# Kernel optimization log

Measured on AMD Instinct MI355X. Metric: run time of the kernel, lower is better.

## Reference

```python
import jax, jax.numpy as jnp
import numpy as np

EPS = 1e-5
POOL_R, POOL_T, SCALE = 5, 7, 0.125  # pool_r, pool_t, 1/pool_stride


def conv_bn_relu(x, W, b, gamma, beta, pad):
    # Conv2d(bias) + BatchNorm2d (training-mode batch stats, biased var) + ReLU
    y = jax.lax.conv_general_dilated(x, W, (1, 1), [(pad, pad), (pad, pad)],
                                     dimension_numbers=('NCHW', 'OIHW', 'NCHW'))
    y = y + b[None, :, None, None]
    mean = y.mean(axis=(0, 2, 3))
    var = y.var(axis=(0, 2, 3))
    y = (y - mean[None, :, None, None]) * jax.lax.rsqrt(var + EPS)[None, :, None, None]
    y = y * gamma[None, :, None, None] + beta[None, :, None, None]
    return jax.nn.relu(y)


def linear_bn_relu(x, W, b, gamma, beta):
    # LinearBlock: Linear + BatchNorm (over batch dim) + ReLU
    y = x @ W.T + b
    mean = y.mean(axis=0)
    var = y.var(axis=0)
    y = (y - mean) * jax.lax.rsqrt(var + EPS) * gamma + beta
    return jax.nn.relu(y)


def _hat_int(x):
    # Antiderivative of the triangular (bilinear) hat kernel at offset x.
    u = jnp.clip(x, -1.0, 1.0)
    return jnp.where(u <= 0, 0.5 * (1.0 + u) ** 2, 0.5 + u - 0.5 * u ** 2)


def prroi_pool(feat, rois, ph, pw, scale):
    # Exact PrRoIPool2D. feat: [B,C,H,W]; rois: [B,N,4] xyxy in image coords.
    # Bilinear interp is a sum of separable hat kernels at integer grid points, so the
    # exact bin integral factorizes into per-axis hat-integral weights Wx, Wy.
    B, C, H, W = feat.shape
    x1, y1, x2, y2 = [rois[..., i] * scale for i in range(4)]
    bw = (x2 - x1) / pw   # [B,N]
    bh = (y2 - y1) / ph
    qx = jnp.arange(pw, dtype=feat.dtype)
    qy = jnp.arange(ph, dtype=feat.dtype)
    xs_lo = x1[..., None] + qx * bw[..., None]   # [B,N,Pw]
    ys_lo = y1[..., None] + qy * bh[..., None]   # [B,N,Ph]
    gw = jnp.arange(W, dtype=feat.dtype)
    gh = jnp.arange(H, dtype=feat.dtype)
    Wx = _hat_int(xs_lo[..., None] + bw[..., None, None] - gw) - _hat_int(xs_lo[..., None] - gw)  # [B,N,Pw,W]
    Wy = _hat_int(ys_lo[..., None] + bh[..., None, None] - gh) - _hat_int(ys_lo[..., None] - gh)  # [B,N,Ph,H]
    out = jnp.einsum('bchw,bnph,bnqw->bncpq', feat, Wy, Wx)
    area = (bw * bh)[:, :, None, None, None]
    return jnp.where(area > 0, out / jnp.maximum(area, 1e-12), 0.0)  # [B,N,C,Ph,Pw]


def _forward(feat1, feat2, bb1, proposals2,
             w_c1r, b_c1r, g_c1r, be_c1r,
             w_c1t, b_c1t, g_c1t, be_c1t,
             w_c2t, b_c2t, g_c2t, be_c2t,
             w_f1r, b_f1r, g_f1r, be_f1r,
             w_f2r, b_f2r, g_f2r, be_f2r,
             w_f1rt, b_f1rt, g_f1rt, be_f1rt,
             w_f2rt, b_f2rt, g_f2rt, be_f2rt,
             w_iou, b_iou):
    S = feat2.shape[0]
    N = proposals2.shape[2]
    # --- get_modulation ---
    c3_r = conv_bn_relu(feat1, w_c1r, b_c1r, g_c1r, be_c1r, 1)
    bb = bb1[0]  # [S,4] xywh -> xyxy
    roi_r = jnp.concatenate([bb[:, :2], bb[:, :2] + bb[:, 2:4]], axis=1)[:, None, :]
    pooled_r = prroi_pool(c3_r, roi_r, POOL_R, POOL_R, SCALE)[:, 0]   # [S,256,5,5]
    m = conv_bn_relu(pooled_r, w_f1r, b_f1r, g_f1r, be_f1r, 0)        # [S,1024,1,1]
    m = conv_bn_relu(m, w_f2r, b_f2r, g_f2r, be_f2r, 0)               # [S,256,1,1]
    modulation = m.reshape(S, -1)                                     # [S,256]
    # --- get_iou_feat ---
    c3_t = conv_bn_relu(conv_bn_relu(feat2, w_c1t, b_c1t, g_c1t, be_c1t, 1),
                        w_c2t, b_c2t, g_c2t, be_c2t, 1)
    # --- predict_iou ---
    c3_t_att = c3_t * modulation[:, :, None, None]
    props = proposals2[0]  # [S,N,4] xywh -> xyxy
    rois_t = jnp.concatenate([props[..., :2], props[..., :2] + props[..., 2:4]], axis=-1)
    pooled_t = prroi_pool(c3_t_att, rois_t, POOL_T, POOL_T, SCALE)    # [S,N,256,7,7]
    x = pooled_t.reshape(S * N, -1)
    x = linear_bn_relu(x, w_f1rt, b_f1rt, g_f1rt, be_f1rt)
    x = linear_bn_relu(x, w_f2rt, b_f2rt, g_f2rt, be_f2rt)
    iou = x @ w_iou.T + b_iou
    return iou.reshape(1, S, N)  # (num_images, num_sequences, num_proposals)


def setup_inputs() -> dict:
    key = jax.random.key(0)
    ks = jax.random.split(key, 8)
    S, C, Hf, Wf, N = 64, 256, 36, 36, 16
    inp = {}
    inp['feat1'] = jax.random.normal(ks[0], (S, C, Hf, Wf), jnp.float32)
    inp['feat2'] = jax.random.normal(ks[1], (S, C, Hf, Wf), jnp.float32)
    xy1 = jax.random.uniform(ks[2], (1, S, 2), minval=20.0, maxval=180.0)
    wh1 = jax.random.uniform(ks[3], (1, S, 2), minval=40.0, maxval=100.0)
    inp['bb1'] = jnp.concatenate([xy1, wh1], axis=-1).astype(jnp.float32)
    xy2 = jax.random.uniform(ks[4], (1, S, N, 2), minval=20.0, maxval=180.0)
    wh2 = jax.random.uniform(ks[5], (1, S, N, 2), minval=40.0, maxval=100.0)
    inp['proposals2'] = jnp.concatenate([xy2, wh2], axis=-1).astype(jnp.float32)

    def kaiming(k, shape):
        fan_in = int(np.prod(shape[1:]))
        return (jax.random.normal(k, shape) * np.sqrt(2.0 / fan_in)).astype(jnp.float32)

    kp = jax.random.split(ks[6], 8)
    specs = [('c1r', (256, C, 3, 3), kp[0]), ('c1t', (256, C, 3, 3), kp[1]),
             ('c2t', (256, 256, 3, 3), kp[2]), ('f1r', (1024, 256, 5, 5), kp[3]),
             ('f2r', (256, 1024, 1, 1), kp[4]), ('f1rt', (1024, 256 * 7 * 7), kp[5]),
             ('f2rt', (1024, 1024), kp[6])]
    for name, shape, k in specs:
        inp['w_' + name] = kaiming(k, shape)
        oc = shape[0]
        inp['b_' + name] = jnp.zeros(oc, jnp.float32)
        inp['g_' + name] = jnp.ones(oc, jnp.float32)
        inp['be_' + name] = jnp.zeros(oc, jnp.float32)
    inp['w_iou'] = kaiming(kp[7], (1, 1024))
    inp['b_iou'] = jnp.zeros(1, jnp.float32)
    return inp


def reference(feat1, feat2, bb1, proposals2,
              w_c1r, b_c1r, g_c1r, be_c1r,
              w_c1t, b_c1t, g_c1t, be_c1t,
              w_c2t, b_c2t, g_c2t, be_c2t,
              w_f1r, b_f1r, g_f1r, be_f1r,
              w_f2r, b_f2r, g_f2r, be_f2r,
              w_f1rt, b_f1rt, g_f1rt, be_f1rt,
              w_f2rt, b_f2rt, g_f2rt, be_f2rt,
              w_iou, b_iou):
    return _forward(feat1, feat2, bb1, proposals2,
                    w_c1r, b_c1r, g_c1r, be_c1r,
                    w_c1t, b_c1t, g_c1t, be_c1t,
                    w_c2t, b_c2t, g_c2t, be_c2t,
                    w_f1r, b_f1r, g_f1r, be_f1r,
                    w_f2r, b_f2r, g_f2r, be_f2r,
                    w_f1rt, b_f1rt, g_f1rt, be_f1rt,
                    w_f2rt, b_f2rt, g_f2rt, be_f2rt,
                    w_iou, b_iou)
```

## Files before the change

### kernel.cpp

```cpp
#include <hip/hip_runtime.h>
#include <cstddef>


typedef _Float16 f16;
typedef __attribute__((ext_vector_type(4))) _Float16 f16x4;
typedef __attribute__((ext_vector_type(8))) _Float16 f16x8;
typedef __attribute__((ext_vector_type(4))) float f32x4;

__device__ __forceinline__ void gload16(const void* g, void* l) {
  __builtin_amdgcn_global_load_lds((const __attribute__((address_space(1))) void*)g,
                                   (__attribute__((address_space(3))) void*)l, 16, 0, 0);
}

#define WAITB(N) asm volatile("s_waitcnt vmcnt(" #N ")\n\ts_barrier" ::: "memory")
#define LGKB()   asm volatile("s_waitcnt lgkmcnt(0)\n\ts_barrier" ::: "memory")

static __device__ __forceinline__ float hat_int(float x) {
  float u = fminf(1.f, fmaxf(-1.f, x));
  float a = 0.5f * (1.f + u) * (1.f + u);
  float b = 0.5f + u - 0.5f * u * u;
  return (u <= 0.f) ? a : b;
}

static __device__ __forceinline__ size_t pk_off(int row, int k, int K) {
  return (size_t)(row >> 7) * ((size_t)K * 128) + (size_t)(k >> 5) * 4096
       + (size_t)((((k >> 3) & 3) * 128 + (row & 127)) * 8 + (k & 7));
}

__global__ void k_zero(float4* __restrict__ p, int n4) {
  int i = blockIdx.x * 256 + threadIdx.x;
  if (i < n4) p[i] = float4{0.f, 0.f, 0.f, 0.f};
}

__global__ void k_border(f16* __restrict__ FT) {
  const int img = blockIdx.x;
  f16* base = FT + (size_t)img * 32 * 1444 * 8;
  for (int i = threadIdx.x; i < 148 * 256; i += 256) {
    int b = i >> 8, c = i & 255;
    int r, cc;
    if (b < 38)       { r = 0;          cc = b; }
    else if (b < 76)  { r = 37;         cc = b - 38; }
    else if (b < 112) { r = b - 76 + 1; cc = 0; }
    else              { r = b - 112 + 1; cc = 37; }
    base[((size_t)(c >> 3) * 1444 + r * 38 + cc) * 8 + (c & 7)] = (f16)0.f;
  }
}

__global__ void k_pad(const float* __restrict__ src, f16* __restrict__ FT) {
  const int img = blockIdx.x, h = blockIdx.y, c = threadIdx.x;
  const float* sp = src + ((size_t)img * 256 + c) * 1296 + h * 36;
  f16* op = FT + (((size_t)img * 32 + (c >> 3)) * 1444 + (h + 1) * 38 + 1) * 8 + (c & 7);
#pragma unroll 4
  for (int w = 0; w < 36; ++w) op[w * 8] = (f16)sp[w];
}

__global__ void k_pad2(const f16* __restrict__ yH, f16* __restrict__ FT,
                       const float* __restrict__ mean, const float* __restrict__ istd,
                       const float* __restrict__ g, const float* __restrict__ be) {
  const int img = blockIdx.x, h = blockIdx.y, c = threadIdx.x;
  const float sc = istd[c] * g[c];
  const float sh = be[c] - mean[c] * sc;
  const f16* sp = yH + ((size_t)img * 1296 + h * 36) * 256 + c;
  f16* op = FT + (((size_t)img * 32 + (c >> 3)) * 1444 + (h + 1) * 38 + 1) * 8 + (c & 7);
#pragma unroll 4
  for (int w = 0; w < 36; ++w) {
    float v = fmaxf(fmaf((float)sp[w * 256], sc, sh), 0.f);
    op[w * 8] = (f16)v;
  }
}

__global__ void k_pack_wc(const float* __restrict__ w, f16* __restrict__ dst) {
  int i = blockIdx.x * 256 + threadIdx.x;
  int oct = i / 294912;
  int r = i - oct * 294912;
  int ks = r >> 12;
  int r2 = r & 4095;
  int koct = r2 >> 10;
  int r3 = r2 & 1023;
  int row = r3 >> 3, kj = r3 & 7;
  int k = ks * 32 + koct * 8 + kj;
  int t = k >> 8, c = k & 255;
  int oc = oct * 128 + row;
  dst[i] = (f16)w[(oc * 256 + c) * 9 + t];
}

__global__ __launch_bounds__(256) void k_packx_h(
    const f16* __restrict__ src, f16* __restrict__ dst, int M, int K) {
  __shared__ f16 sT[128][264];
  const int k0 = blockIdx.x * 256, r0 = blockIdx.y * 128;
  const int t = threadIdx.x;
  const int rl = t >> 5, kk = (t & 31) * 8;
  for (int rnd = 0; rnd < 16; ++rnd) {
    const int row_l = rl + rnd * 8;
    const int row = r0 + row_l;
    if (row < M) {
      f16x8 v = *reinterpret_cast<const f16x8*>(src + (size_t)row * K + k0 + kk);
      *reinterpret_cast<f16x8*>(&sT[row_l][kk]) = v;
    }
  }
  __syncthreads();
  const size_t base = (size_t)(r0 >> 7) * ((size_t)K * 128) + (size_t)(k0 >> 5) * 4096;
#pragma unroll
  for (int cs = 0; cs < 8; ++cs) {
#pragma unroll
    for (int half = 0; half < 2; ++half) {
      const int e = half * 256 + t;
      const int koct = e >> 7, row_l = e & 127;
      if (r0 + row_l < M) {
        f16x8 v = *reinterpret_cast<const f16x8*>(&sT[row_l][cs * 32 + koct * 8]);
        *reinterpret_cast<f16x8*>(dst + base + (size_t)cs * 4096 + e * 8) = v;
      }
    }
  }
}

__global__ __launch_bounds__(256) void k_packx_f(
    const float* __restrict__ src, f16* __restrict__ dst, int M, int K) {
  __shared__ f16 sT[128][264];
  const int k0 = blockIdx.x * 256, r0 = blockIdx.y * 128;
  const int t = threadIdx.x;
  const int rl = t >> 5, kk = (t & 31) * 8;
  for (int rnd = 0; rnd < 16; ++rnd) {
    const int row_l = rl + rnd * 8;
    const int row = r0 + row_l;
    if (row < M) {
      const float4* sp = reinterpret_cast<const float4*>(src + (size_t)row * K + k0 + kk);
      float4 a = sp[0], b = sp[1];
      f16* o = &sT[row_l][kk];
      o[0] = (f16)a.x; o[1] = (f16)a.y; o[2] = (f16)a.z; o[3] = (f16)a.w;
      o[4] = (f16)b.x; o[5] = (f16)b.y; o[6] = (f16)b.z; o[7] = (f16)b.w;
    }
  }
  __syncthreads();
  const size_t base = (size_t)(r0 >> 7) * ((size_t)K * 128) + (size_t)(k0 >> 5) * 4096;
#pragma unroll
  for (int cs = 0; cs < 8; ++cs) {
#pragma unroll
    for (int half = 0; half < 2; ++half) {
      const int e = half * 256 + t;
      const int koct = e >> 7, row_l = e & 127;
      if (r0 + row_l < M) {
        f16x8 v = *reinterpret_cast<const f16x8*>(&sT[row_l][cs * 32 + koct * 8]);
        *reinterpret_cast<f16x8*>(dst + base + (size_t)cs * 4096 + e * 8) = v;
      }
    }
  }
}

__global__ __launch_bounds__(256) void k_conv_mfma(
    const f16* __restrict__ Wpk, const f16* __restrict__ FT2,
    const float* __restrict__ bias, f16* __restrict__ yH) {
  __shared__ f16x8 sA[1536];
  __shared__ f16x8 sB[1536];
  const int bid = blockIdx.x;
  const int orig = (bid & 7) * 176 + (bid >> 3);
  const int img = orig / 22;
  const int rem = orig - img * 22;
  const int oct = rem / 11;
  const int pt  = rem - oct * 11;
  const int m0 = oct * 128;
  const int p0 = pt * 128;
  const int tid = threadIdx.x;
  const int lane = tid & 63;
  const int wv = tid >> 6;
  const int wr = wv >> 1, wc = wv & 1;

  const f16* aBase = Wpk + (size_t)oct * 294912 + wv * 1024 + lane * 8;
  const f16* ftImg = FT2 + (size_t)img * 32 * 1444 * 8;
  int pos0 = p0 + lane;
  int pc0 = min(pos0, 1295);
  int pc1 = min(pos0 + 64, 1295);
  int pb0 = (pc0 / 36) * 38 + (pc0 % 36);
  int pb1 = (pc1 / 36) * 38 + (pc1 % 36);

  const int loff = wv * 2048 + lane * 16;

  auto stage = [&](int buf, int ks) {
    const int t = ks >> 3;
    const int dy = t / 3, dx = t - dy * 3;
    const int cs = ks & 7;
    const int dyx = dy * 38 + dx;
    char* lA = (char*)sA + buf * 8192 + loff;
    char* lB = (char*)sB + buf * 8192 + loff;
    const f16* ap = aBase + (size_t)ks * 4096;
    const f16* bp = ftImg + ((size_t)(cs * 4 + wv) * 1444 + dyx) * 8;
    gload16(ap, lA);
    gload16(ap + 512, lA + 1024);
    gload16(bp + pb0 * 8, lB);
    gload16(bp + pb1 * 8, lB + 1024);
  };

  f32x4 acc[4][4] = {};
  const int fidxA = ((lane >> 4) << 7) + wr * 64 + (lane & 15);
  const int fidxB = ((lane >> 4) << 7) + wc * 64 + (lane & 15);

  stage(0, 0); stage(1, 1); stage(2, 2);
  int cur = 0;
  for (int ks = 0; ks < 72; ++ks) {
    const int r = 71 - ks;
    if (r >= 2)      WAITB(8);
    else if (r == 1) WAITB(4);
    else             WAITB(0);
    const int base = cur * 512;
    f16x8 af[4], bf[4];
#pragma unroll
    for (int i = 0; i < 4; ++i) {
      af[i] = sA[base + fidxA + i * 16];
      bf[i] = sB[base + fidxB + i * 16];
    }
#pragma unroll
    for (int i = 0; i < 4; ++i)
#pragma unroll
      for (int j = 0; j < 4; ++j)
        acc[i][j] = __builtin_amdgcn_mfma_f32_16x16x32_f16(af[i], bf[j], acc[i][j], 0, 0, 0);
    LGKB();
    if (ks + 3 < 72) stage(cur, ks + 3);
    cur = (cur == 2) ? 0 : cur + 1;
  }

  const int colb = p0 + wc * 64 + (lane & 15);
  const int rowb = m0 + wr * 64 + ((lane >> 4) << 2);
  f16* yb = yH + (size_t)img * 1296 * 256;
#pragma unroll
  for (int i = 0; i < 4; ++i) {
    const int oc0 = rowb + i * 16;
    float b0 = bias[oc0], b1 = bias[oc0 + 1], b2 = bias[oc0 + 2], b3 = bias[oc0 + 3];
#pragma unroll
    for (int j = 0; j < 4; ++j) {
      const int col = colb + j * 16;
      if (col < 1296) {
        f16x4 v;
        v[0] = (f16)(acc[i][j][0] + b0);
        v[1] = (f16)(acc[i][j][1] + b1);
        v[2] = (f16)(acc[i][j][2] + b2);
        v[3] = (f16)(acc[i][j][3] + b3);
        *reinterpret_cast<f16x4*>(yb + (size_t)col * 256 + oc0) = v;
      }
    }
  }
}

__global__ __launch_bounds__(256) void k_gemm_f16pk(
    const f16* __restrict__ Apk, const f16* __restrict__ Bpk,
    float* __restrict__ part, int K, int Nout, int stepsPerZ, int mrows) {
  __shared__ f16x8 sA[1536];
  __shared__ f16x8 sB[1536];
  const int nt = blockIdx.x, mt = blockIdx.y, z = blockIdx.z;
  const int tid = threadIdx.x;
  const int lane = tid & 63;
  const int wv = tid >> 6;
  const int wr = wv >> 1, wc = wv & 1;

  const f16* aC = Apk + (size_t)mt * K * 128 + wv * 1024 + lane * 8;
  const f16* bC = Bpk + (size_t)nt * K * 128 + wv * 1024 + lane * 8;
  const int loff = wv * 2048 + lane * 16;

  auto stage = [&](int buf, int ks) {
    char* lA = (char*)sA + buf * 8192 + loff;
    char* lB = (char*)sB + buf * 8192 + loff;
    const f16* ap = aC + (size_t)ks * 4096;
    const f16* bp = bC + (size_t)ks * 4096;
    gload16(ap, lA);
    gload16(ap + 512, lA + 1024);
    gload16(bp, lB);
    gload16(bp + 512, lB + 1024);
  };

  f32x4 acc[4][4] = {};
  const int fidxA = ((lane >> 4) << 7) + wr * 64 + (lane & 15);
  const int fidxB = ((lane >> 4) << 7) + wc * 64 + (lane & 15);

  const int ks0 = z * stepsPerZ;
  stage(0, ks0); stage(1, ks0 + 1); stage(2, ks0 + 2);
  int cur = 0;
  for (int i = 0; i < stepsPerZ; ++i) {
    const int r = stepsPerZ - 1 - i;
    if (r >= 2)      WAITB(8);
    else if (r == 1) WAITB(4);
    else             WAITB(0);
    const int base = cur * 512;
    f16x8 af[4], bf[4];
#pragma unroll
    for (int j = 0; j < 4; ++j) {
      af[j] = sA[base + fidxA + j * 16];
      bf[j] = sB[base + fidxB + j * 16];
    }
#pragma unroll
    for (int ii = 0; ii < 4; ++ii)
#pragma unroll
      for (int jj = 0; jj < 4; ++jj)
        acc[ii][jj] = __builtin_amdgcn_mfma_f32_16x16x32_f16(af[ii], bf[jj], acc[ii][jj], 0, 0, 0);
    LGKB();
    if (i + 3 < stepsPerZ) stage(cur, ks0 + i + 3);
    cur = (cur == 2) ? 0 : cur + 1;
  }

  const size_t zoff = (size_t)z * mrows * Nout;
  const int colb = nt * 128 + wc * 64 + (lane & 15);
  const int rowb = mt * 128 + wr * 64 + ((lane >> 4) << 2);
#pragma unroll
  for (int i = 0; i < 4; ++i)
#pragma unroll
    for (int j = 0; j < 4; ++j)
#pragma unroll
      for (int r = 0; r < 4; ++r)
        part[zoff + (size_t)(rowb + i * 16 + r) * Nout + colb + j * 16] = acc[i][j][r];
}

__global__ void k_reduce(const float* __restrict__ part, const float* __restrict__ bias,
                         float* __restrict__ out, int mrows, int Mout, int Nout, int sk) {
  int i = blockIdx.x * 256 + threadIdx.x;
  if (i >= Mout * Nout) return;
  int row = i / Nout, col = i - row * Nout;
  float s = bias[col];
  for (int z = 0; z < sk; ++z)
    s += part[(size_t)z * mrows * Nout + (size_t)row * Nout + col];
  out[i] = s;
}

__global__ void k_chan_stats_hwc(const f16* __restrict__ yH,
                                 float* __restrict__ psum, float* __restrict__ psq) {
  const int z = blockIdx.x, c = threadIdx.x;
  const f16* p = yH + (size_t)z * 256 * 256 + c;
  float s = 0.f, ss = 0.f;
#pragma unroll 4
  for (int i = 0; i < 256; ++i) {
    float v = (float)p[(size_t)i * 256];
    s += v; ss += v * v;
  }
  psum[z * 256 + c] = s;
  psq[z * 256 + c] = ss;
}

__global__ void k_chan_stats_hwc_final(const float* __restrict__ psum,
                                       const float* __restrict__ psq,
                                       float* __restrict__ mean, float* __restrict__ istd) {
  const int c = threadIdx.x;
  float s = 0.f, ss = 0.f;
  for (int z = 0; z < 324; ++z) { s += psum[z * 256 + c]; ss += psq[z * 256 + c]; }
  float m = s * (1.f / 82944.f);
  float var = ss * (1.f / 82944.f) - m * m;
  mean[c] = m;
  istd[c] = rsqrtf(var + 1e-5f);
}

__global__ void k_wxy(const float* __restrict__ rois, int ntot, int P,
                      float* __restrict__ Wx, float* __restrict__ Wy,
                      float* __restrict__ area,
                      int* __restrict__ HLO, int* __restrict__ HCNT,
                      int* __restrict__ WLO) {
  int idx = blockIdx.x * blockDim.x + threadIdx.x;
  if (idx >= ntot) return;
  float rx = rois[idx * 4 + 0], ry = rois[idx * 4 + 1];
  float rw = rois[idx * 4 + 2], rh = rois[idx * 4 + 3];
  float x1 = rx * 0.125f, y1 = ry * 0.125f;
  float x2 = (rx + rw) * 0.125f, y2 = (ry + rh) * 0.125f;
  float bw = (x2 - x1) / P, bh = (y2 - y1) / P;
  area[idx] = bw * bh;
  int hlo = max(0, (int)ceilf(y1 - 1.f));
  int hhi = min(35, (int)floorf(y2 + 1.f));
  HLO[idx] = hlo;
  HCNT[idx] = max(0, hhi - hlo + 1);
  for (int q = 0; q < P; ++q) {
    float xlo = x1 + q * bw, ylo = y1 + q * bh;
    WLO[idx * P + q] = min(31, max(0, (int)ceilf(xlo - 1.f)));
    for (int g = 0; g < 36; ++g) {
      float fg = (float)g;
      Wx[(idx * P + q) * 36 + g] = hat_int(xlo + bw - fg) - hat_int(xlo - fg);
      Wy[(idx * P + q) * 36 + g] = hat_int(ylo + bh - fg) - hat_int(ylo - fg);
    }
  }
}

template <int P, bool MOD>
__global__ __launch_bounds__(256) void k_pool(
    const f16* __restrict__ feat, const float* __restrict__ Wx,
    const float* __restrict__ Wy, const float* __restrict__ area,
    const int* __restrict__ HLO, const int* __restrict__ HCNT,
    const int* __restrict__ WLO,
    const float* __restrict__ mean, const float* __restrict__ istd,
    const float* __restrict__ g, const float* __restrict__ be,
    const float* __restrict__ mod, f16* __restrict__ out, int N) {
  const int s = blockIdx.x, n = blockIdx.y;
  const int idx = s * N + n;
  const int c = threadIdx.x;
  constexpr int KD = P * P * 256;
  __shared__ f16 sOut[KD];
  __shared__ float sWx[P * 36], sWy[P * 36];
  __shared__ int sWLO[P];
  __shared__ int sH[2];
  for (int i = threadIdx.x; i < P * 36; i += 256) {
    sWx[i] = Wx[(size_t)idx * P * 36 + i];
    sWy[i] = Wy[(size_t)idx * P * 36 + i];
  }
  if (threadIdx.x < P) sWLO[threadIdx.x] = WLO[idx * P + threadIdx.x];
  if (threadIdx.x == 0) { sH[0] = HLO[idx]; sH[1] = HCNT[idx]; }
  __syncthreads();
  const float sc = istd[c] * g[c];
  const float sh = be[c] - mean[c] * sc;
  const f16* f = feat + (size_t)s * 1296 * 256 + c;
  float o[P][P] = {};
  const int hlo = sH[0], hcnt = sH[1];
  for (int hh = 0; hh < hcnt; ++hh) {
    const int h = hlo + hh;
    const f16* rp = f + (size_t)h * 36 * 256;
    float colsum[P];
#pragma unroll
    for (int q = 0; q < P; ++q) {
      const int w0 = sWLO[q];
      const f16* wp = rp + (size_t)w0 * 256;
      float v = 0.f;
#pragma unroll
      for (int j = 0; j < 5; ++j) {
        float x = fmaxf(fmaf((float)wp[j * 256], sc, sh), 0.f);
        v = fmaf(sWx[q * 36 + w0 + j], x, v);
      }
      colsum[q] = v;
    }
#pragma unroll
    for (int p = 0; p < P; ++p) {
      const float wy = sWy[p * 36 + h];
      if (wy != 0.f) {
#pragma unroll
        for (int q = 0; q < P; ++q) o[p][q] = fmaf(wy, colsum[q], o[p][q]);
      }
    }
  }
  float a = area[idx];
  float inv = (a > 0.f) ? 1.f / fmaxf(a, 1e-12f) : 0.f;
  float msc = MOD ? (mod[s * 256 + c] * inv) : inv;
  const int kbase = c * (P * P);
#pragma unroll
  for (int p = 0; p < P; ++p)
#pragma unroll
    for (int q = 0; q < P; ++q)
      sOut[kbase + p * P + q] = (f16)(o[p][q] * msc);
  __syncthreads();
  f16* op = out + (size_t)idx * KD;
  for (int j = threadIdx.x; j < KD; j += 256) op[j] = sOut[j];
}

__global__ void k_fc_stats_part(const float* __restrict__ y, int M, int Nf, int rpz,
                                float* __restrict__ psum, float* __restrict__ psq) {
  int col = blockIdx.x * 256 + threadIdx.x;
  int z = blockIdx.y;
  if (col >= Nf) return;
  int r0 = z * rpz;
  int r1 = min(M, r0 + rpz);
  float s = 0.f, ss = 0.f;
  for (int m = r0; m < r1; ++m) {
    float v = y[(size_t)m * Nf + col];
    s += v; ss += v * v;
  }
  psum[(size_t)z * Nf + col] = s;
  psq[(size_t)z * Nf + col] = ss;
}

__global__ void k_fc_stats_final(const float* __restrict__ psum, const float* __restrict__ psq,
                                 int nz, int Nf, int M,
                                 float* __restrict__ mean, float* __restrict__ istd) {
  int col = blockIdx.x * 256 + threadIdx.x;
  if (col >= Nf) return;
  float s = 0.f, ss = 0.f;
  for (int z = 0; z < nz; ++z) {
    s += psum[(size_t)z * Nf + col];
    ss += psq[(size_t)z * Nf + col];
  }
  float mu = s / (float)M;
  float var = ss / (float)M - mu * mu;
  mean[col] = mu;
  istd[col] = rsqrtf(var + 1e-5f);
}

__global__ void k_fc_bn_relu(float* __restrict__ y, const float* __restrict__ mean,
                             const float* __restrict__ istd, const float* __restrict__ g,
                             const float* __restrict__ be, int total, int Nf) {
  int i = blockIdx.x * 256 + threadIdx.x;
  if (i >= total) return;
  int col = i % Nf;
  float sc = istd[col] * g[col];
  float sh = be[col] - mean[col] * sc;
  y[i] = fmaxf(fmaf(y[i], sc, sh), 0.f);
}

__global__ void k_fc_bn_relu_pk(const float* __restrict__ y, const float* __restrict__ mean,
                                const float* __restrict__ istd, const float* __restrict__ g,
                                const float* __restrict__ be, f16* __restrict__ xpk,
                                int total, int Nf) {
  int i = blockIdx.x * 256 + threadIdx.x;
  if (i >= total) return;
  int row = i / Nf, col = i - row * Nf;
  float sc = istd[col] * g[col];
  float sh = be[col] - mean[col] * sc;
  float v = fmaxf(fmaf(y[i], sc, sh), 0.f);
  xpk[pk_off(row, col, Nf)] = (f16)v;
}

__global__ void k_iou(const float* __restrict__ x, const float* __restrict__ w,
                      const float* __restrict__ b, float* __restrict__ out) {
  const int r = blockIdx.x, tid = threadIdx.x;
  float s = 0.f;
  for (int k = tid; k < 1024; k += 256) s = fmaf(x[(size_t)r * 1024 + k], w[k], s);
  __shared__ float red[256];
  red[tid] = s;
  __syncthreads();
  for (int o = 128; o > 0; o >>= 1) {
    if (tid < o) red[tid] += red[tid + o];
    __syncthreads();
  }
  if (tid == 0) out[r] = red[0] + b[0];
}

static const size_t O_A      = 0;
static const size_t O_POOLT  = 12000000;
static const size_t O_PSUM   = 13000000;
static const size_t O_PSQ    = 13065536;
static const size_t O_WPK2RT = 16000000;
static const size_t O_POOLR  = 18500000;
static const size_t O_WPK2R  = 20000000;
static const size_t O_FT     = 21233664;
static const size_t O_X2PK   = 21233664 + 6422528;
static const size_t O_WC     = 33062912;
static const size_t O_WPK1RT = 33357824;
static const size_t O_WPK1R  = 39780352;
static const size_t O_PRPK   = 43057152;
static const size_t O_Y1     = 43466752;
static const size_t O_Y2     = 44515328;
static const size_t O_MOD    = 45563904;
static const size_t O_WXR    = 45580288;
static const size_t O_WYR    = 45591808;
static const size_t O_ARR    = 45603328;
static const size_t O_WXT    = 45603392;
static const size_t O_WYT    = 45861440;
static const size_t O_ART    = 46119488;
static const size_t O_MEAN   = 46120512;
static const size_t O_ISTD   = 46121536;
static const size_t O_X1PK   = 46122560;
static const size_t O_META   = 46188096;
static const size_t O_PSC    = 46197760;

extern "C" void kernel_launch(void* const* d_in, const int* in_sizes, int n_in,
                              void* d_out, int out_size, void* d_ws, size_t ws_size,
                              hipStream_t stream) {
  (void)in_sizes; (void)n_in; (void)out_size; (void)ws_size;
  const float* feat1  = (const float*)d_in[0];
  const float* feat2  = (const float*)d_in[1];
  const float* bb1    = (const float*)d_in[2];
  const float* props  = (const float*)d_in[3];
  const float* w_c1r  = (const float*)d_in[4];
  const float* b_c1r  = (const float*)d_in[5];
  const float* g_c1r  = (const float*)d_in[6];
  const float* be_c1r = (const float*)d_in[7];
  const float* w_c1t  = (const float*)d_in[8];
  const float* b_c1t  = (const float*)d_in[9];
  const float* g_c1t  = (const float*)d_in[10];
  const float* be_c1t = (const float*)d_in[11];
  const float* w_c2t  = (const float*)d_in[12];
  const float* b_c2t  = (const float*)d_in[13];
  const float* g_c2t  = (const float*)d_in[14];
  const float* be_c2t = (const float*)d_in[15];
  const float* w_f1r  = (const float*)d_in[16];
  const float* b_f1r  = (const float*)d_in[17];
  const float* g_f1r  = (const float*)d_in[18];
  const float* be_f1r = (const float*)d_in[19];
  const float* w_f2r  = (const float*)d_in[20];
  const float* b_f2r  = (const float*)d_in[21];
  const float* g_f2r  = (const float*)d_in[22];
  const float* be_f2r = (const float*)d_in[23];
  const float* w_f1rt = (const float*)d_in[24];
  const float* b_f1rt = (const float*)d_in[25];
  const float* g_f1rt = (const float*)d_in[26];
  const float* be_f1rt= (const float*)d_in[27];
  const float* w_f2rt = (const float*)d_in[28];
  const float* b_f2rt = (const float*)d_in[29];
  const float* g_f2rt = (const float*)d_in[30];
  const float* be_f2rt= (const float*)d_in[31];
  const float* w_iou  = (const float*)d_in[32];
  const float* b_iou  = (const float*)d_in[33];

  float* ws    = (float*)d_ws;
  f16*   AH    = (f16*)(ws + O_A);
  float* PART  = ws + O_A;
  f16*   POOLT = (f16*)(ws + O_POOLT);
  float* PSUM  = ws + O_PSUM;
  float* PSQ   = ws + O_PSQ;
  f16*   WPK2RT= (f16*)(ws + O_WPK2RT);
  f16*   POOLR = (f16*)(ws + O_POOLR);
  f16*   WPK2R = (f16*)(ws + O_WPK2R);
  f16*   FT2   = (f16*)(ws + O_FT);
  f16*   PHPK  = FT2;
  f16*   X2PK  = (f16*)(ws + O_X2PK);
  f16*   WC    = (f16*)(ws + O_WC);
  f16*   WPK1RT= (f16*)(ws + O_WPK1RT);
  f16*   WPK1R = (f16*)(ws + O_WPK1R);
  f16*   PRPK  = (f16*)(ws + O_PRPK);
  float* Y1    = ws + O_Y1;
  float* Y2    = ws + O_Y2;
  float* MODp  = ws + O_MOD;
  float* WXR   = ws + O_WXR;
  float* WYR   = ws + O_WYR;
  float* ARR   = ws + O_ARR;
  float* WXT   = ws + O_WXT;
  float* WYT   = ws + O_WYT;
  float* ART   = ws + O_ART;
  float* MEAN  = ws + O_MEAN;
  float* ISTD  = ws + O_ISTD;
  f16*   X1PK  = (f16*)(ws + O_X1PK);
  int*   META  = (int*)(ws + O_META);
  float* PSUMC = ws + O_PSC;
  float* PSQC  = ws + O_PSC + 82944;
  int* HLOR = META;
  int* HCNTR= META + 64;
  int* WLOR = META + 128;
  int* HLOT = META + 448;
  int* HCNTT= META + 1472;
  int* WLOT = META + 2496;

  k_border<<<64, 256, 0, stream>>>(FT2);
  k_pack_wc<<<2304, 256, 0, stream>>>(w_c1r, WC);
  k_pad<<<dim3(64, 36), 256, 0, stream>>>(feat1, FT2);
  k_conv_mfma<<<1408, 256, 0, stream>>>(WC, FT2, b_c1r, AH);
  k_chan_stats_hwc<<<324, 256, 0, stream>>>(AH, PSUMC, PSQC);
  k_chan_stats_hwc_final<<<1, 256, 0, stream>>>(PSUMC, PSQC, MEAN, ISTD);

  k_wxy<<<1, 64, 0, stream>>>(bb1, 64, 5, WXR, WYR, ARR, HLOR, HCNTR, WLOR);
  k_zero<<<400, 256, 0, stream>>>((float4*)PRPK, 102400);
  k_pool<5, false><<<dim3(64, 1), 256, 0, stream>>>(
      AH, WXR, WYR, ARR, HLOR, HCNTR, WLOR, MEAN, ISTD, g_c1r, be_c1r, nullptr, POOLR, 1);
  k_packx_h<<<dim3(25, 1), 256, 0, stream>>>(POOLR, PRPK, 64, 6400);

  k_packx_f<<<dim3(25, 8), 256, 0, stream>>>(w_f1r, WPK1R, 1024, 6400);
  k_gemm_f16pk<<<dim3(8, 1, 8), 256, 0, stream>>>(PRPK, WPK1R, PART, 6400, 1024, 25, 128);
  k_reduce<<<256, 256, 0, stream>>>(PART, b_f1r, Y1, 128, 64, 1024, 8);
  k_fc_stats_part<<<dim3(4, 8), 256, 0, stream>>>(Y1, 64, 1024, 8, PSUM, PSQ);
  k_fc_stats_final<<<4, 256, 0, stream>>>(PSUM, PSQ, 8, 1024, 64, MEAN, ISTD);
  k_zero<<<64, 256, 0, stream>>>((float4*)X1PK, 16384);
  k_fc_bn_relu_pk<<<256, 256, 0, stream>>>(Y1, MEAN, ISTD, g_f1r, be_f1r, X1PK, 64 * 1024, 1024);

  k_packx_f<<<dim3(4, 2), 256, 0, stream>>>(w_f2r, WPK2R, 256, 1024);
  k_gemm_f16pk<<<dim3(2, 1, 4), 256, 0, stream>>>(X1PK, WPK2R, PART, 1024, 256, 8, 128);
  k_reduce<<<64, 256, 0, stream>>>(PART, b_f2r, MODp, 128, 64, 256, 4);
  k_fc_stats_part<<<dim3(1, 8), 256, 0, stream>>>(MODp, 64, 256, 8, PSUM, PSQ);
  k_fc_stats_final<<<1, 256, 0, stream>>>(PSUM, PSQ, 8, 256, 64, MEAN, ISTD);
  k_fc_bn_relu<<<64, 256, 0, stream>>>(MODp, MEAN, ISTD, g_f2r, be_f2r, 64 * 256, 256);

  k_pack_wc<<<2304, 256, 0, stream>>>(w_c1t, WC);
  k_pad<<<dim3(64, 36), 256, 0, stream>>>(feat2, FT2);
  k_conv_mfma<<<1408, 256, 0, stream>>>(WC, FT2, b_c1t, AH);
  k_chan_stats_hwc<<<324, 256, 0, stream>>>(AH, PSUMC, PSQC);
  k_chan_stats_hwc_final<<<1, 256, 0, stream>>>(PSUMC, PSQC, MEAN, ISTD);
  k_pad2<<<dim3(64, 36), 256, 0, stream>>>(AH, FT2, MEAN, ISTD, g_c1t, be_c1t);

  k_pack_wc<<<2304, 256, 0, stream>>>(w_c2t, WC);
  k_conv_mfma<<<1408, 256, 0, stream>>>(WC, FT2, b_c2t, AH);
  k_chan_stats_hwc<<<324, 256, 0, stream>>>(AH, PSUMC, PSQC);
  k_chan_stats_hwc_final<<<1, 256, 0, stream>>>(PSUMC, PSQC, MEAN, ISTD);

  k_wxy<<<16, 64, 0, stream>>>(props, 1024, 7, WXT, WYT, ART, HLOT, HCNTT, WLOT);
  k_pool<7, true><<<dim3(64, 16), 256, 0, stream>>>(
      AH, WXT, WYT, ART, HLOT, HCNTT, WLOT, MEAN, ISTD, g_c2t, be_c2t, MODp, POOLT, 16);
  k_packx_h<<<dim3(49, 8), 256, 0, stream>>>(POOLT, PHPK, 1024, 12544);

  k_packx_f<<<dim3(49, 8), 256, 0, stream>>>(w_f1rt, WPK1RT, 1024, 12544);
  k_gemm_f16pk<<<dim3(8, 8, 8), 256, 0, stream>>>(PHPK, WPK1RT, PART, 12544, 1024, 49, 1024);
  k_reduce<<<4096, 256, 0, stream>>>(PART, b_f1rt, Y1, 1024, 1024, 1024, 8);
  k_fc_stats_part<<<dim3(4, 64), 256, 0, stream>>>(Y1, 1024, 1024, 16, PSUM, PSQ);
  k_fc_stats_final<<<4, 256, 0, stream>>>(PSUM, PSQ, 64, 1024, 1024, MEAN, ISTD);
  k_fc_bn_relu_pk<<<4096, 256, 0, stream>>>(Y1, MEAN, ISTD, g_f1rt, be_f1rt, X2PK, 1024 * 1024, 1024);

  k_packx_f<<<dim3(4, 8), 256, 0, stream>>>(w_f2rt, WPK2RT, 1024, 1024);
  k_gemm_f16pk<<<dim3(8, 8, 4), 256, 0, stream>>>(X2PK, WPK2RT, PART, 1024, 1024, 8, 1024);
  k_reduce<<<4096, 256, 0, stream>>>(PART, b_f2rt, Y2, 1024, 1024, 1024, 4);
  k_fc_stats_part<<<dim3(4, 64), 256, 0, stream>>>(Y2, 1024, 1024, 16, PSUM, PSQ);
  k_fc_stats_final<<<4, 256, 0, stream>>>(PSUM, PSQ, 64, 1024, 1024, MEAN, ISTD);
  k_fc_bn_relu<<<4096, 256, 0, stream>>>(Y2, MEAN, ISTD, g_f2rt, be_f2rt, 1024 * 1024, 1024);

  k_iou<<<1024, 256, 0, stream>>>(Y2, w_iou, b_iou, (float*)d_out);
}
```

Before: 951.0 us.

## Stage conv epilogue through LDS, raise MFMA priority, fuse reduce with stats

The conv epilogue now writes biased f16 results into a padded LDS tile, then stores 16-byte vectors per output row instead of scattered 8-byte stores. Both MFMA loops wrap the matrix multiplies in s_setprio to favour the compute wave over loads. The split-K reduce kernel is merged with the FC column-stats kernel, so each output is read once and partial sums and squares come out of the same pass. The fused reduce uses fewer, longer-running blocks, which lowers parallelism in that step.

```diff
diff --git a/kernel.cpp b/kernel.cpp
--- a/kernel.cpp
+++ b/kernel.cpp
@@ -3,7 +3,6 @@
 
 
 typedef _Float16 f16;
-typedef __attribute__((ext_vector_type(4))) _Float16 f16x4;
 typedef __attribute__((ext_vector_type(8))) _Float16 f16x8;
 typedef __attribute__((ext_vector_type(4))) float f32x4;
 
@@ -150,8 +149,9 @@
 __global__ __launch_bounds__(256) void k_conv_mfma(
     const f16* __restrict__ Wpk, const f16* __restrict__ FT2,
     const float* __restrict__ bias, f16* __restrict__ yH) {
-  __shared__ f16x8 sA[1536];
-  __shared__ f16x8 sB[1536];
+  __shared__ __align__(16) char smem[49152];
+  f16x8* sA = (f16x8*)smem;
+  f16x8* sB = (f16x8*)(smem + 24576);
   const int bid = blockIdx.x;
   const int orig = (bid & 7) * 176 + (bid >> 3);
   const int img = orig / 22;
@@ -208,35 +208,45 @@
       af[i] = sA[base + fidxA + i * 16];
       bf[i] = sB[base + fidxB + i * 16];
     }
+    __builtin_amdgcn_s_setprio(1);
 #pragma unroll
     for (int i = 0; i < 4; ++i)
 #pragma unroll
       for (int j = 0; j < 4; ++j)
         acc[i][j] = __builtin_amdgcn_mfma_f32_16x16x32_f16(af[i], bf[j], acc[i][j], 0, 0, 0);
+    __builtin_amdgcn_s_setprio(0);
     LGKB();
     if (ks + 3 < 72) stage(cur, ks + 3);
     cur = (cur == 2) ? 0 : cur + 1;
   }
 
-  const int colb = p0 + wc * 64 + (lane & 15);
-  const int rowb = m0 + wr * 64 + ((lane >> 4) << 2);
-  f16* yb = yH + (size_t)img * 1296 * 256;
+  __syncthreads();
+  f16* sE = (f16*)smem;
+  const int ocl = wr * 64 + ((lane >> 4) << 2);
 #pragma unroll
   for (int i = 0; i < 4; ++i) {
-    const int oc0 = rowb + i * 16;
+    const int oc0 = m0 + ocl + i * 16;
     float b0 = bias[oc0], b1 = bias[oc0 + 1], b2 = bias[oc0 + 2], b3 = bias[oc0 + 3];
 #pragma unroll
     for (int j = 0; j < 4; ++j) {
-      const int col = colb + j * 16;
-      if (col < 1296) {
-        f16x4 v;
-        v[0] = (f16)(acc[i][j][0] + b0);
-        v[1] = (f16)(acc[i][j][1] + b1);
-        v[2] = (f16)(acc[i][j][2] + b2);
-        v[3] = (f16)(acc[i][j][3] + b3);
-        *reinterpret_cast<f16x4*>(yb + (size_t)col * 256 + oc0) = v;
-      }
-    }
+      f16* e = &sE[(wc * 64 + j * 16 + (lane & 15)) * 136 + ocl + i * 16];
+      e[0] = (f16)(acc[i][j][0] + b0);
+      e[1] = (f16)(acc[i][j][1] + b1);
+      e[2] = (f16)(acc[i][j][2] + b2);
+      e[3] = (f16)(acc[i][j][3] + b3);
+    }
+  }
+  __syncthreads();
+  f16* yb = yH + (size_t)img * 1296 * 256 + m0;
+#pragma unroll
+  for (int it = 0; it < 8; ++it) {
+    const int e = (it * 256 + tid) * 8;
+    const int row = e >> 7;
+    const int oc = e & 127;
+    const int col = p0 + row;
+    if (col < 1296)
+      *reinterpret_cast<f16x8*>(yb + (size_t)col * 256 + oc) =
+        *reinterpret_cast<const f16x8*>(&sE[row * 136 + oc]);
   }
 }
 
@@ -285,11 +295,13 @@
       af[j] = sA[base + fidxA + j * 16];
       bf[j] = sB[base + fidxB + j * 16];
     }
+    __builtin_amdgcn_s_setprio(1);
 #pragma unroll
     for (int ii = 0; ii < 4; ++ii)
 #pragma unroll
       for (int jj = 0; jj < 4; ++jj)
         acc[ii][jj] = __builtin_amdgcn_mfma_f32_16x16x32_f16(af[ii], bf[jj], acc[ii][jj], 0, 0, 0);
+    __builtin_amdgcn_s_setprio(0);
     LGKB();
     if (i + 3 < stepsPerZ) stage(cur, ks0 + i + 3);
     cur = (cur == 2) ? 0 : cur + 1;
@@ -307,15 +319,24 @@
         part[zoff + (size_t)(rowb + i * 16 + r) * Nout + colb + j * 16] = acc[i][j][r];
 }
 
-__global__ void k_reduce(const float* __restrict__ part, const float* __restrict__ bias,
-                         float* __restrict__ out, int mrows, int Mout, int Nout, int sk) {
-  int i = blockIdx.x * 256 + threadIdx.x;
-  if (i >= Mout * Nout) return;
-  int row = i / Nout, col = i - row * Nout;
-  float s = bias[col];
-  for (int z = 0; z < sk; ++z)
-    s += part[(size_t)z * mrows * Nout + (size_t)row * Nout + col];
-  out[i] = s;
+__global__ void k_reduce_stats(const float* __restrict__ part, const float* __restrict__ bias,
+                               float* __restrict__ out, int mrows, int Mout, int Nout,
+                               int sk, int rpz,
+                               float* __restrict__ psum, float* __restrict__ psq) {
+  const int col = blockIdx.x * 256 + threadIdx.x;
+  const int z = blockIdx.y;
+  const float b = bias[col];
+  float s = 0.f, ss = 0.f;
+  const int r0 = z * rpz, r1 = min(Mout, r0 + rpz);
+  for (int m = r0; m < r1; ++m) {
+    float v = b;
+    for (int zz = 0; zz < sk; ++zz)
+      v += part[(size_t)zz * mrows * Nout + (size_t)m * Nout + col];
+    out[(size_t)m * Nout + col] = v;
+    s += v; ss += v * v;
+  }
+  psum[(size_t)z * Nout + col] = s;
+  psq[(size_t)z * Nout + col] = ss;
 }
 
 __global__ void k_chan_stats_hwc(const f16* __restrict__ yH,
@@ -438,22 +459,6 @@
   __syncthreads();
   f16* op = out + (size_t)idx * KD;
   for (int j = threadIdx.x; j < KD; j += 256) op[j] = sOut[j];
-}
-
-__global__ void k_fc_stats_part(const float* __restrict__ y, int M, int Nf, int rpz,
-                                float* __restrict__ psum, float* __restrict__ psq) {
-  int col = blockIdx.x * 256 + threadIdx.x;
-  int z = blockIdx.y;
-  if (col >= Nf) return;
-  int r0 = z * rpz;
-  int r1 = min(M, r0 + rpz);
-  float s = 0.f, ss = 0.f;
-  for (int m = r0; m < r1; ++m) {
-    float v = y[(size_t)m * Nf + col];
-    s += v; ss += v * v;
-  }
-  psum[(size_t)z * Nf + col] = s;
-  psq[(size_t)z * Nf + col] = ss;
 }
 
 __global__ void k_fc_stats_final(const float* __restrict__ psum, const float* __restrict__ psq,
@@ -631,16 +636,14 @@
 
   k_packx_f<<<dim3(25, 8), 256, 0, stream>>>(w_f1r, WPK1R, 1024, 6400);
   k_gemm_f16pk<<<dim3(8, 1, 8), 256, 0, stream>>>(PRPK, WPK1R, PART, 6400, 1024, 25, 128);
-  k_reduce<<<256, 256, 0, stream>>>(PART, b_f1r, Y1, 128, 64, 1024, 8);
-  k_fc_stats_part<<<dim3(4, 8), 256, 0, stream>>>(Y1, 64, 1024, 8, PSUM, PSQ);
+  k_reduce_stats<<<dim3(4, 8), 256, 0, stream>>>(PART, b_f1r, Y1, 128, 64, 1024, 8, 8, PSUM, PSQ);
   k_fc_stats_final<<<4, 256, 0, stream>>>(PSUM, PSQ, 8, 1024, 64, MEAN, ISTD);
   k_zero<<<64, 256, 0, stream>>>((float4*)X1PK, 16384);
   k_fc_bn_relu_pk<<<256, 256, 0, stream>>>(Y1, MEAN, ISTD, g_f1r, be_f1r, X1PK, 64 * 1024, 1024);
 
   k_packx_f<<<dim3(4, 2), 256, 0, stream>>>(w_f2r, WPK2R, 256, 1024);
   k_gemm_f16pk<<<dim3(2, 1, 4), 256, 0, stream>>>(X1PK, WPK2R, PART, 1024, 256, 8, 128);
-  k_reduce<<<64, 256, 0, stream>>>(PART, b_f2r, MODp, 128, 64, 256, 4);
-  k_fc_stats_part<<<dim3(1, 8), 256, 0, stream>>>(MODp, 64, 256, 8, PSUM, PSQ);
+  k_reduce_stats<<<dim3(1, 8), 256, 0, stream>>>(PART, b_f2r, MODp, 128, 64, 256, 4, 8, PSUM, PSQ);
   k_fc_stats_final<<<1, 256, 0, stream>>>(PSUM, PSQ, 8, 256, 64, MEAN, ISTD);
   k_fc_bn_relu<<<64, 256, 0, stream>>>(MODp, MEAN, ISTD, g_f2r, be_f2r, 64 * 256, 256);
 
@@ -663,15 +666,13 @@
 
   k_packx_f<<<dim3(49, 8), 256, 0, stream>>>(w_f1rt, WPK1RT, 1024, 12544);
   k_gemm_f16pk<<<dim3(8, 8, 8), 256, 0, stream>>>(PHPK, WPK1RT, PART, 12544, 1024, 49, 1024);
-  k_reduce<<<4096, 256, 0, stream>>>(PART, b_f1rt, Y1, 1024, 1024, 1024, 8);
-  k_fc_stats_part<<<dim3(4, 64), 256, 0, stream>>>(Y1, 1024, 1024, 16, PSUM, PSQ);
+  k_reduce_stats<<<dim3(4, 64), 256, 0, stream>>>(PART, b_f1rt, Y1, 1024, 1024, 1024, 8, 16, PSUM, PSQ);
   k_fc_stats_final<<<4, 256, 0, stream>>>(PSUM, PSQ, 64, 1024, 1024, MEAN, ISTD);
   k_fc_bn_relu_pk<<<4096, 256, 0, stream>>>(Y1, MEAN, ISTD, g_f1rt, be_f1rt, X2PK, 1024 * 1024, 1024);
 
   k_packx_f<<<dim3(4, 8), 256, 0, stream>>>(w_f2rt, WPK2RT, 1024, 1024);
   k_gemm_f16pk<<<dim3(8, 8, 4), 256, 0, stream>>>(X2PK, WPK2RT, PART, 1024, 1024, 8, 1024);
-  k_reduce<<<4096, 256, 0, stream>>>(PART, b_f2rt, Y2, 1024, 1024, 1024, 4);
-  k_fc_stats_part<<<dim3(4, 64), 256, 0, stream>>>(Y2, 1024, 1024, 16, PSUM, PSQ);
+  k_reduce_stats<<<dim3(4, 64), 256, 0, stream>>>(PART, b_f2rt, Y2, 1024, 1024, 1024, 4, 16, PSUM, PSQ);
   k_fc_stats_final<<<4, 256, 0, stream>>>(PSUM, PSQ, 64, 1024, 1024, MEAN, ISTD);
   k_fc_bn_relu<<<4096, 256, 0, stream>>>(Y2, MEAN, ISTD, g_f2rt, be_f2rt, 1024 * 1024, 1024);
 
```

New measurement: 974.3 us. 2.5% more time.
